# Kernel optimization log

Measured on AMD Instinct MI355X. Metric: run time of the kernel, lower is better.

## Reference

```python
import jax, jax.numpy as jnp
import numpy as np

N, E, IN_DIM, HID, OUT = 50000, 800000, 256, 128, 128
EPS_BN = 1e-5
EPS_NORM = 1e-12


def leaky(x):
    return jnp.where(x >= 0, x, 0.2 * x)


def batchnorm(x, gamma, beta):
    # training-mode BatchNorm1d over node dimension
    mean = jnp.mean(x, axis=0)
    var = jnp.var(x, axis=0)
    return gamma * (x - mean) * jax.lax.rsqrt(var + EPS_BN) + beta


def sage_conv(x, src, dst, W_l, b_l, W_r):
    # PyG SAGEConv (mean aggr): lin_l(mean_{j->i} x_j) + lin_r(x_i)
    msg = x[src]  # [E, D] gather
    agg = jax.ops.segment_sum(msg, dst, num_segments=N)
    cnt = jax.ops.segment_sum(jnp.ones((E,), x.dtype), dst, num_segments=N)
    agg = agg / jnp.maximum(cnt, 1.0)[:, None]
    return agg @ W_l + b_l + x @ W_r


def setup_inputs() -> dict:
    key = jax.random.key(0)
    ks = jax.random.split(key, 16)
    s = lambda fan_in: (2.0 / fan_in) ** 0.5
    return {
        "x": jax.random.normal(ks[0], (N, IN_DIM), jnp.float32),
        "edge_index": jax.random.randint(ks[1], (2, E), 0, N),
        "W_in": jax.random.normal(ks[2], (IN_DIM, HID), jnp.float32) * s(IN_DIM),
        "b_in": jnp.zeros((HID,), jnp.float32),
        "g1": jnp.ones((HID,), jnp.float32),
        "be1": jnp.zeros((HID,), jnp.float32),
        "Wl1": jax.random.normal(ks[3], (HID, HID), jnp.float32) * s(HID),
        "bl1": jnp.zeros((HID,), jnp.float32),
        "Wr1": jax.random.normal(ks[4], (HID, HID), jnp.float32) * s(HID),
        "Wl2": jax.random.normal(ks[5], (HID, OUT), jnp.float32) * s(HID),
        "bl2": jnp.zeros((OUT,), jnp.float32),
        "Wr2": jax.random.normal(ks[6], (HID, OUT), jnp.float32) * s(HID),
        "Wskip": jax.random.normal(ks[7], (HID, OUT), jnp.float32) * s(HID),
        "bskip": jnp.zeros((OUT,), jnp.float32),
        "g2": jnp.ones((OUT,), jnp.float32),
        "be2": jnp.zeros((OUT,), jnp.float32),
    }


def reference(x, edge_index, W_in, b_in, g1, be1, Wl1, bl1, Wr1, Wl2, bl2, Wr2, Wskip, bskip, g2, be2):
    src, dst = edge_index[0], edge_index[1]
    h = batchnorm(leaky(x @ W_in + b_in), g1, be1)
    skip = h
    h1 = leaky(sage_conv(h, src, dst, Wl1, bl1, Wr1))  # dropout = identity (eval)
    h2 = sage_conv(h1, src, dst, Wl2, bl2, Wr2)
    out = h2 + (skip @ Wskip + bskip)
    out = batchnorm(out, g2, be2)
    norm = jnp.sqrt(jnp.sum(out * out, axis=1, keepdims=True))
    return out / jnp.maximum(norm, EPS_NORM)
```

## Files before the change

kernel.cpp:

```cpp
#include <hip/hip_runtime.h>
#include <math.h>

#define N_NODES 50000
#define N_EDGES 800000
#define IN_DIM 256
#define HID 128
#define ZPITCH 384

typedef unsigned short u16;
typedef u16 u16x8 __attribute__((ext_vector_type(8)));
typedef u16 u16x2 __attribute__((ext_vector_type(2)));
typedef __bf16 bf16x8 __attribute__((ext_vector_type(8)));
typedef float f32x4 __attribute__((ext_vector_type(4)));

union F8 { u16x8 u; bf16x8 h; };

__device__ __forceinline__ u16 f2b(float f) {
    unsigned u = __builtin_bit_cast(unsigned, f);
    u = (u + 0x7FFFu + ((u >> 16) & 1u)) >> 16;
    return (u16)u;
}
__device__ __forceinline__ float b2f(u16 h) {
    unsigned u = ((unsigned)h) << 16;
    return __builtin_bit_cast(float, u);
}

template<int A_F32>
__device__ __forceinline__ F8 load_a(const void* base, size_t row, int P, int koff)
{
    F8 r;
    if (A_F32) {
        const float* p = (const float*)base + row * P + koff;
        float4 f0 = *reinterpret_cast<const float4*>(p);
        float4 f1 = *reinterpret_cast<const float4*>(p + 4);
        r.h[0] = (__bf16)f0.x; r.h[1] = (__bf16)f0.y;
        r.h[2] = (__bf16)f0.z; r.h[3] = (__bf16)f0.w;
        r.h[4] = (__bf16)f1.x; r.h[5] = (__bf16)f1.y;
        r.h[6] = (__bf16)f1.z; r.h[7] = (__bf16)f1.w;
    } else {
        r.u = *reinterpret_cast<const u16x8*>((const u16*)base + row * P + koff);
    }
    return r;
}

template<int LEAKY, int STATS, int OUT_BF16, int A_F32, int NC>
__global__ __launch_bounds__(512, 3) void gemm_mfma(
    int M, const void* __restrict__ A, int P,
    const u16* __restrict__ Wf,
    const float* __restrict__ bias0, const float* __restrict__ bias1,
    void* __restrict__ Cout, int CP,
    float* __restrict__ stats)
{
    __shared__ u16 Bs[NC * 4096];

    const int t   = threadIdx.x;
    const int w   = t >> 6;
    const int l   = t & 63;
    const int l15 = l & 15;
    const int lg  = l >> 4;
    const int rb  = blockIdx.x * 128 + w * 16;

    int r0 = rb + l15;
    size_t r0c = (size_t)(r0 < M ? r0 : M - 1);
    const int ko = lg * 8;

    F8 a[NC];
#pragma unroll
    for (int c = 0; c < NC; ++c) a[c] = load_a<A_F32>(A, r0c, P, c * 32 + ko);

#pragma unroll
    for (int i = 0; i < NC; ++i) {
        int idx = i * 512 + t;
        reinterpret_cast<u16x8*>(Bs)[idx] = reinterpret_cast<const u16x8*>(Wf)[idx];
    }
    __syncthreads();

    f32x4 acc[8];
#pragma unroll
    for (int j = 0; j < 8; ++j) acc[j] = 0.0f;

#pragma unroll
    for (int c = 0; c < NC; ++c) {
#pragma unroll
        for (int j = 0; j < 8; ++j) {
            F8 b;
            b.u = reinterpret_cast<const u16x8*>(Bs)[(c * 8 + j) * 64 + l];
            acc[j] = __builtin_amdgcn_mfma_f32_16x16x32_bf16(a[c].h, b.h, acc[j], 0, 0, 0);
        }
    }

    float bias_j[8];
#pragma unroll
    for (int j = 0; j < 8; ++j) {
        float bb = bias0[16 * j + l15];
        if (bias1) bb += bias1[16 * j + l15];
        bias_j[j] = bb;
    }

    float csum[8], csq[8];
#pragma unroll
    for (int j = 0; j < 8; ++j) { csum[j] = 0.f; csq[j] = 0.f; }

    {
        int rbase = rb + lg * 4;
#pragma unroll
        for (int r = 0; r < 4; ++r) {
            int row = rbase + r;
            bool ok = row < M;
#pragma unroll
            for (int j = 0; j < 8; ++j) {
                float y = acc[j][r] + bias_j[j];
                if (LEAKY) y = (y >= 0.f) ? y : 0.2f * y;
                if (ok) {
                    if (OUT_BF16)
                        ((u16*)Cout)[(size_t)row * CP + 16 * j + l15] = f2b(y);
                    else
                        ((float*)Cout)[(size_t)row * CP + 16 * j + l15] = y;
                    if (STATS) { csum[j] += y; csq[j] += y * y; }
                }
            }
        }
    }

    if (STATS) {
        __shared__ float sred[256];
        if (t < 256) sred[t] = 0.f;
        __syncthreads();
#pragma unroll
        for (int j = 0; j < 8; ++j) {
            float s = csum[j];
            float q = csq[j];
            s += __shfl_xor(s, 16); s += __shfl_xor(s, 32);
            q += __shfl_xor(q, 16); q += __shfl_xor(q, 32);
            if (lg == 0) {
                atomicAdd(&sred[16 * j + l15], s);
                atomicAdd(&sred[128 + 16 * j + l15], q);
            }
        }
        __syncthreads();
        if (t < 256) atomicAdd(&stats[t], sred[t]);
    }
}

__global__ __launch_bounds__(256) void conv_w(const float* s0, const float* s1, const float* s2,
                                              const float* sc0, const float* sc1, const float* sc2,
                                              int rows_each, u16* __restrict__ dst, int nchunks)
{
    int tid = blockIdx.x * 256 + threadIdx.x;
    if (tid >= nchunks * 512) return;
    int c   = tid >> 9;
    int j   = (tid >> 6) & 7;
    int l   = tid & 63;
    int l15 = l & 15, lg = l >> 4;

    int srow0 = c * 32;
    int si    = srow0 / rows_each;
    const float* S  = (si == 0) ? s0 : (si == 1) ? s1 : s2;
    const float* SC = (si == 0) ? sc0 : (si == 1) ? sc1 : sc2;
    int rbase = srow0 - si * rows_each + lg * 8;
    int col   = 16 * j + l15;

    u16x8 o;
#pragma unroll
    for (int i = 0; i < 8; ++i) {
        float v = S[(size_t)(rbase + i) * HID + col];
        if (SC) v *= SC[rbase + i];
        o[i] = f2b(v);
    }
    reinterpret_cast<u16x8*>(dst)[tid] = o;
}

__global__ void bias_fold(const float* __restrict__ b0, const float* __restrict__ b1,
                          const float* __restrict__ W0, const float* __restrict__ W1,
                          const float* __restrict__ sh, float* __restrict__ outb)
{
    int j = threadIdx.x;
    float acc = b0[j] + (b1 ? b1[j] : 0.f);
    for (int i = 0; i < HID; ++i) {
        float w = W0[(size_t)i * HID + j] + (W1 ? W1[(size_t)i * HID + j] : 0.f);
        acc = fmaf(sh[i], w, acc);
    }
    outb[j] = acc;
}

__global__ void bn_params(const float* __restrict__ stats,
                          const float* __restrict__ gamma,
                          const float* __restrict__ beta,
                          float* __restrict__ scale,
                          float* __restrict__ shift, float invn)
{
    int j = threadIdx.x;
    float mean = stats[j] * invn;
    float var  = stats[128 + j] * invn - mean * mean;
    var = fmaxf(var, 0.f);
    float sc = gamma[j] / sqrtf(var + 1e-5f);
    scale[j] = sc;
    shift[j] = beta[j] - mean * sc;
}

__global__ __launch_bounds__(256) void edge_count(const int* __restrict__ dst, int* __restrict__ cnt)
{
    int e = blockIdx.x * 256 + threadIdx.x;
    if (e < N_EDGES) atomicAdd(&cnt[dst[e]], 1);
}

__global__ __launch_bounds__(256) void scan_block(const int* __restrict__ cnt,
                                                  int* __restrict__ excl,
                                                  int* __restrict__ bsum, int n)
{
    __shared__ int sh[256];
    int t = threadIdx.x;
    int i = blockIdx.x * 256 + t;
    int v = (i < n) ? cnt[i] : 0;
    sh[t] = v;
    __syncthreads();
#pragma unroll
    for (int off = 1; off < 256; off <<= 1) {
        int x = (t >= off) ? sh[t - off] : 0;
        __syncthreads();
        sh[t] += x;
        __syncthreads();
    }
    if (i < n) excl[i] = sh[t] - v;
    if (t == 255) bsum[blockIdx.x] = sh[255];
}

__global__ __launch_bounds__(256) void scan_bsum(int* __restrict__ bsum, int nb)
{
    __shared__ int sh[256];
    int t = threadIdx.x;
    int v = (t < nb) ? bsum[t] : 0;
    sh[t] = v;
    __syncthreads();
#pragma unroll
    for (int off = 1; off < 256; off <<= 1) {
        int x = (t >= off) ? sh[t - off] : 0;
        __syncthreads();
        sh[t] += x;
        __syncthreads();
    }
    if (t < nb) bsum[t] = sh[t] - v;
}

__global__ __launch_bounds__(256) void scan_add(int* __restrict__ row_ptr,
                                                int* __restrict__ fillrp,
                                                const int* __restrict__ bsum, int n)
{
    int i = blockIdx.x * 256 + threadIdx.x;
    if (i < n) {
        int v = row_ptr[i] + bsum[i >> 8];
        row_ptr[i] = v;
        fillrp[i]  = v;
    }
    if (i == 0) row_ptr[n] = N_EDGES;
}

#define FILL_EPB 4096
__global__ __launch_bounds__(256) void edge_fill_part(const int* __restrict__ src,
                                                      const int* __restrict__ dst,
                                                      int* __restrict__ fillrp,
                                                      int* __restrict__ col_idx)
{
    const int range = blockIdx.x & 7;
    const int base  = (blockIdx.x >> 3) * FILL_EPB;
    const int lo = range * 6250, hi = lo + 6250;
#pragma unroll
    for (int k = 0; k < FILL_EPB / 256; ++k) {
        int e = base + k * 256 + threadIdx.x;
        if (e < N_EDGES) {
            int d = dst[e];
            if (d >= lo && d < hi) {
                int pos = atomicAdd(&fillrp[d], 1);
                col_idx[pos] = src[e];
            }
        }
    }
}

__global__ __launch_bounds__(256) void spmm_mean(const int* __restrict__ row_ptr,
                                                 const int* __restrict__ col_idx,
                                                 const u16* __restrict__ Z_in,
                                                 u16* __restrict__ Z_out)
{
    int node = blockIdx.x * 4 + (threadIdx.x >> 6);
    if (node >= N_NODES) return;
    int lane = threadIdx.x & 63;
    int beg = row_ptr[node];
    int end = row_ptr[node + 1];

    float sx = 0.f, sy = 0.f;
    int e = beg;
    for (; e + 4 <= end; e += 4) {
        int c0 = col_idx[e], c1 = col_idx[e + 1], c2 = col_idx[e + 2], c3 = col_idx[e + 3];
        u16x2 v0 = *reinterpret_cast<const u16x2*>(Z_in + (size_t)c0 * ZPITCH + lane * 2);
        u16x2 v1 = *reinterpret_cast<const u16x2*>(Z_in + (size_t)c1 * ZPITCH + lane * 2);
        u16x2 v2 = *reinterpret_cast<const u16x2*>(Z_in + (size_t)c2 * ZPITCH + lane * 2);
        u16x2 v3 = *reinterpret_cast<const u16x2*>(Z_in + (size_t)c3 * ZPITCH + lane * 2);
        sx += (b2f(v0[0]) + b2f(v1[0])) + (b2f(v2[0]) + b2f(v3[0]));
        sy += (b2f(v0[1]) + b2f(v1[1])) + (b2f(v2[1]) + b2f(v3[1]));
    }
    for (; e < end; ++e) {
        int c = col_idx[e];
        u16x2 v = *reinterpret_cast<const u16x2*>(Z_in + (size_t)c * ZPITCH + lane * 2);
        sx += b2f(v[0]); sy += b2f(v[1]);
    }
    float inv = 1.f / fmaxf((float)(end - beg), 1.f);
    u16x2 r; r[0] = f2b(sx * inv); r[1] = f2b(sy * inv);
    *reinterpret_cast<u16x2*>(Z_out + (size_t)node * ZPITCH + lane * 2) = r;
}

__global__ __launch_bounds__(256) void bn_rownorm(float* __restrict__ out,
                                                  const float* __restrict__ scale,
                                                  const float* __restrict__ shift)
{
    int row = blockIdx.x * 4 + (threadIdx.x >> 6);
    if (row >= N_NODES) return;
    int lane = threadIdx.x & 63;
    float2 v  = *reinterpret_cast<const float2*>(&out[(size_t)row * HID + lane * 2]);
    float2 sc = *reinterpret_cast<const float2*>(&scale[lane * 2]);
    float2 sh = *reinterpret_cast<const float2*>(&shift[lane * 2]);
    float y0 = v.x * sc.x + sh.x;
    float y1 = v.y * sc.y + sh.y;
    float ss = y0 * y0 + y1 * y1;
#pragma unroll
    for (int m = 1; m < 64; m <<= 1) ss += __shfl_xor(ss, m);
    float inv = 1.f / fmaxf(sqrtf(ss), 1e-12f);
    float2 r = {y0 * inv, y1 * inv};
    *reinterpret_cast<float2*>(&out[(size_t)row * HID + lane * 2]) = r;
}

extern "C" void kernel_launch(void* const* d_in, const int* in_sizes, int n_in,
                              void* d_out, int out_size, void* d_ws, size_t ws_size,
                              hipStream_t stream)
{
    const float* x     = (const float*)d_in[0];
    const int*   ei    = (const int*)d_in[1];
    const float* W_in  = (const float*)d_in[2];
    const float* b_in  = (const float*)d_in[3];
    const float* g1    = (const float*)d_in[4];
    const float* be1   = (const float*)d_in[5];
    const float* Wl1   = (const float*)d_in[6];
    const float* bl1   = (const float*)d_in[7];
    const float* Wr1   = (const float*)d_in[8];
    const float* Wl2   = (const float*)d_in[9];
    const float* bl2   = (const float*)d_in[10];
    const float* Wr2   = (const float*)d_in[11];
    const float* Wskip = (const float*)d_in[12];
    const float* bskip = (const float*)d_in[13];
    const float* g2    = (const float*)d_in[14];
    const float* be2   = (const float*)d_in[15];
    float* out = (float*)d_out;

    char* ws = (char*)d_ws;
    u16*  Z  = (u16*)ws;
    char* zzone = ws + 38400000;
    float* stats = (float*)zzone;
    int*   icnt  = (int*)(zzone + 2048);
    size_t zsz   = 2048 + (size_t)N_NODES * 4;
    int*   row_ptr = (int*)(zzone + zsz);
    int*   fillrp  = (int*)(zzone + zsz + 200064);
    int*   bsum    = (int*)(zzone + zsz + 400128);
    int*   col_idx = (int*)(zzone + zsz + 400128 + 1024);
    float* bnc     = (float*)(zzone + zsz + 400128 + 1024 + (size_t)N_EDGES * 4);
    u16* WfA = (u16*)((char*)bnc + 4096);
    u16* WfB = WfA + 8 * 4096;
    u16* WfC = WfB + 8 * 4096;

    hipMemsetAsync(zzone, 0, zsz, stream);

    const int* srcp = ei;
    const int* dstp = ei + N_EDGES;

    float* scale1 = bnc;
    float* shift1 = bnc + 128;
    float* scale2 = bnc + 256;
    float* shift2 = bnc + 384;
    float* b1eff  = bnc + 512;
    float* b2eff  = bnc + 640;

    conv_w<<<16, 256, 0, stream>>>(W_in, nullptr, nullptr, nullptr, nullptr, nullptr,
                                   256, WfA, 8);

    const int NB = (N_NODES + 255) / 256;
    edge_count<<<(N_EDGES + 255) / 256, 256, 0, stream>>>(dstp, icnt);
    scan_block<<<NB, 256, 0, stream>>>(icnt, row_ptr, bsum, N_NODES);
    scan_bsum<<<1, 256, 0, stream>>>(bsum, NB);
    scan_add<<<NB, 256, 0, stream>>>(row_ptr, fillrp, bsum, N_NODES);
    edge_fill_part<<<((N_EDGES + FILL_EPB - 1) / FILL_EPB) * 8, 256, 0, stream>>>(
        srcp, dstp, fillrp, col_idx);

    const int GB = (N_NODES + 127) / 128;

    gemm_mfma<1, 1, 1, 1, 8><<<GB, 512, 0, stream>>>(
        N_NODES, x, IN_DIM, WfA, b_in, nullptr, Z + 128, ZPITCH, stats);
    bn_params<<<1, 128, 0, stream>>>(stats, g1, be1, scale1, shift1, 1.f / N_NODES);

    conv_w<<<16, 256, 0, stream>>>(Wl1, Wr1, nullptr, scale1, scale1, nullptr,
                                   128, WfB, 8);
    conv_w<<<24, 256, 0, stream>>>(Wl2, Wskip, Wr2, nullptr, scale1, nullptr,
                                   128, WfC, 12);
    bias_fold<<<1, 128, 0, stream>>>(bl1, nullptr, Wl1, Wr1, shift1, b1eff);
    bias_fold<<<1, 128, 0, stream>>>(bl2, bskip, Wskip, nullptr, shift1, b2eff);

    spmm_mean<<<(N_NODES + 3) / 4, 256, 0, stream>>>(row_ptr, col_idx, Z + 128, Z);
    gemm_mfma<1, 0, 1, 0, 8><<<GB, 512, 0, stream>>>(
        N_NODES, Z, ZPITCH, WfB, b1eff, nullptr, Z + 256, ZPITCH, nullptr);

    spmm_mean<<<(N_NODES + 3) / 4, 256, 0, stream>>>(row_ptr, col_idx, Z + 256, Z);
    gemm_mfma<0, 1, 0, 0, 12><<<GB, 512, 0, stream>>>(
        N_NODES, Z, ZPITCH, WfC, b2eff, nullptr, out, HID, stats + 256);

    bn_params<<<1, 128, 0, stream>>>(stats + 256, g2, be2, scale2, shift2, 1.f / N_NODES);
    bn_rownorm<<<(N_NODES + 3) / 4, 256, 0, stream>>>(out, scale2, shift2);
}
```

Baseline: 276.2 us.

## Double GEMM rows per wave, async LDS weight load, prefetch A and B fragments

The MFMA GEMM now computes 32 rows per wave (256 per block) so each B fragment read from LDS feeds two MFMAs. Weights are copied into LDS with global_load_lds so they skip registers, A chunks are prefetched a few steps ahead, and the next B fragments are double-buffered in registers. The unused bias1 argument is removed. This raises register pressure (launch bounds lowered to 2 blocks per CU) and halves the grid, which may reduce occupancy and latency hiding.

```diff
diff --git a/kernel.cpp b/kernel.cpp
--- a/kernel.cpp
+++ b/kernel.cpp
@@ -13,6 +13,9 @@
 typedef __bf16 bf16x8 __attribute__((ext_vector_type(8)));
 typedef float f32x4 __attribute__((ext_vector_type(4)));
 
+#define AS1 __attribute__((address_space(1)))
+#define AS3 __attribute__((address_space(3)))
+
 union F8 { u16x8 u; bf16x8 h; };
 
 __device__ __forceinline__ u16 f2b(float f) {
@@ -25,29 +28,46 @@
     return __builtin_bit_cast(float, u);
 }
 
+template<int A_F32> struct ARaw;
+template<> struct ARaw<0> { u16x8 v; };
+template<> struct ARaw<1> { float4 f0, f1; };
+
 template<int A_F32>
-__device__ __forceinline__ F8 load_a(const void* base, size_t row, int P, int koff)
-{
-    F8 r;
-    if (A_F32) {
-        const float* p = (const float*)base + row * P + koff;
-        float4 f0 = *reinterpret_cast<const float4*>(p);
-        float4 f1 = *reinterpret_cast<const float4*>(p + 4);
-        r.h[0] = (__bf16)f0.x; r.h[1] = (__bf16)f0.y;
-        r.h[2] = (__bf16)f0.z; r.h[3] = (__bf16)f0.w;
-        r.h[4] = (__bf16)f1.x; r.h[5] = (__bf16)f1.y;
-        r.h[6] = (__bf16)f1.z; r.h[7] = (__bf16)f1.w;
-    } else {
-        r.u = *reinterpret_cast<const u16x8*>((const u16*)base + row * P + koff);
-    }
+__device__ __forceinline__ ARaw<A_F32> load_raw(const void* base, size_t row, int P, int koff);
+template<>
+__device__ __forceinline__ ARaw<0> load_raw<0>(const void* base, size_t row, int P, int koff) {
+    ARaw<0> r;
+    r.v = *reinterpret_cast<const u16x8*>((const u16*)base + row * P + koff);
     return r;
 }
+template<>
+__device__ __forceinline__ ARaw<1> load_raw<1>(const void* base, size_t row, int P, int koff) {
+    ARaw<1> r;
+    const float* p = (const float*)base + row * P + koff;
+    r.f0 = *reinterpret_cast<const float4*>(p);
+    r.f1 = *reinterpret_cast<const float4*>(p + 4);
+    return r;
+}
+
+template<int A_F32>
+__device__ __forceinline__ F8 to_frag(const ARaw<A_F32>& r);
+template<>
+__device__ __forceinline__ F8 to_frag<0>(const ARaw<0>& r) { F8 f; f.u = r.v; return f; }
+template<>
+__device__ __forceinline__ F8 to_frag<1>(const ARaw<1>& r) {
+    F8 f;
+    f.h[0] = (__bf16)r.f0.x; f.h[1] = (__bf16)r.f0.y;
+    f.h[2] = (__bf16)r.f0.z; f.h[3] = (__bf16)r.f0.w;
+    f.h[4] = (__bf16)r.f1.x; f.h[5] = (__bf16)r.f1.y;
+    f.h[6] = (__bf16)r.f1.z; f.h[7] = (__bf16)r.f1.w;
+    return f;
+}
 
 template<int LEAKY, int STATS, int OUT_BF16, int A_F32, int NC>
-__global__ __launch_bounds__(512, 3) void gemm_mfma(
+__global__ __launch_bounds__(512, 2) void gemm_mfma(
     int M, const void* __restrict__ A, int P,
     const u16* __restrict__ Wf,
-    const float* __restrict__ bias0, const float* __restrict__ bias1,
+    const float* __restrict__ bias0,
     void* __restrict__ Cout, int CP,
     float* __restrict__ stats)
 {
@@ -58,58 +78,84 @@
     const int l   = t & 63;
     const int l15 = l & 15;
     const int lg  = l >> 4;
-    const int rb  = blockIdx.x * 128 + w * 16;
+    const int rb  = blockIdx.x * 256 + w * 32;
 
     int r0 = rb + l15;
+    int r1 = r0 + 16;
     size_t r0c = (size_t)(r0 < M ? r0 : M - 1);
+    size_t r1c = (size_t)(r1 < M ? r1 : M - 1);
     const int ko = lg * 8;
-
-    F8 a[NC];
-#pragma unroll
-    for (int c = 0; c < NC; ++c) a[c] = load_a<A_F32>(A, r0c, P, c * 32 + ko);
 
 #pragma unroll
     for (int i = 0; i < NC; ++i) {
         int idx = i * 512 + t;
-        reinterpret_cast<u16x8*>(Bs)[idx] = reinterpret_cast<const u16x8*>(Wf)[idx];
-    }
+        __builtin_amdgcn_global_load_lds(
+            (const AS1 void*)(Wf + (size_t)idx * 8),
+            (AS3 void*)(Bs + (size_t)idx * 8), 16, 0, 0);
+    }
+
+    constexpr int D = (NC < 4) ? NC : 4;
+    ARaw<A_F32> a0[NC], a1[NC];
+#pragma unroll
+    for (int c = 0; c < D; ++c) {
+        a0[c] = load_raw<A_F32>(A, r0c, P, c * 32 + ko);
+        a1[c] = load_raw<A_F32>(A, r1c, P, c * 32 + ko);
+    }
+
     __syncthreads();
 
-    f32x4 acc[8];
-#pragma unroll
-    for (int j = 0; j < 8; ++j) acc[j] = 0.0f;
+    f32x4 acc[2][8];
+#pragma unroll
+    for (int m = 0; m < 2; ++m)
+#pragma unroll
+        for (int j = 0; j < 8; ++j) acc[m][j] = 0.0f;
+
+    F8 b[8], nb[8];
+#pragma unroll
+    for (int j = 0; j < 8; ++j)
+        b[j].u = *reinterpret_cast<const u16x8*>(Bs + (size_t)(j * 64 + l) * 8);
 
 #pragma unroll
     for (int c = 0; c < NC; ++c) {
+        if (c + D < NC) {
+            a0[c + D] = load_raw<A_F32>(A, r0c, P, (c + D) * 32 + ko);
+            a1[c + D] = load_raw<A_F32>(A, r1c, P, (c + D) * 32 + ko);
+        }
+        if (c + 1 < NC) {
+#pragma unroll
+            for (int j = 0; j < 8; ++j)
+                nb[j].u = *reinterpret_cast<const u16x8*>(
+                    Bs + (size_t)(((c + 1) * 8 + j) * 64 + l) * 8);
+        }
+        F8 fa0 = to_frag<A_F32>(a0[c]);
+        F8 fa1 = to_frag<A_F32>(a1[c]);
 #pragma unroll
         for (int j = 0; j < 8; ++j) {
-            F8 b;
-            b.u = reinterpret_cast<const u16x8*>(Bs)[(c * 8 + j) * 64 + l];
-            acc[j] = __builtin_amdgcn_mfma_f32_16x16x32_bf16(a[c].h, b.h, acc[j], 0, 0, 0);
-        }
+            acc[0][j] = __builtin_amdgcn_mfma_f32_16x16x32_bf16(fa0.h, b[j].h, acc[0][j], 0, 0, 0);
+            acc[1][j] = __builtin_amdgcn_mfma_f32_16x16x32_bf16(fa1.h, b[j].h, acc[1][j], 0, 0, 0);
+        }
+#pragma unroll
+        for (int j = 0; j < 8; ++j) b[j] = nb[j];
     }
 
     float bias_j[8];
 #pragma unroll
-    for (int j = 0; j < 8; ++j) {
-        float bb = bias0[16 * j + l15];
-        if (bias1) bb += bias1[16 * j + l15];
-        bias_j[j] = bb;
-    }
+    for (int j = 0; j < 8; ++j) bias_j[j] = bias0[16 * j + l15];
 
     float csum[8], csq[8];
 #pragma unroll
     for (int j = 0; j < 8; ++j) { csum[j] = 0.f; csq[j] = 0.f; }
 
-    {
-        int rbase = rb + lg * 4;
+#pragma unroll
+    for (int m = 0; m < 2; ++m) {
+        int rbase = rb + m * 16 + lg * 4;
 #pragma unroll
         for (int r = 0; r < 4; ++r) {
             int row = rbase + r;
             bool ok = row < M;
 #pragma unroll
             for (int j = 0; j < 8; ++j) {
-                float y = acc[j][r] + bias_j[j];
+                float y = acc[m][j][r] + bias_j[j];
                 if (LEAKY) y = (y >= 0.f) ? y : 0.2f * y;
                 if (ok) {
                     if (OUT_BF16)
@@ -389,10 +435,10 @@
     edge_fill_part<<<((N_EDGES + FILL_EPB - 1) / FILL_EPB) * 8, 256, 0, stream>>>(
         srcp, dstp, fillrp, col_idx);
 
-    const int GB = (N_NODES + 127) / 128;
+    const int GB = (N_NODES + 255) / 256;
 
     gemm_mfma<1, 1, 1, 1, 8><<<GB, 512, 0, stream>>>(
-        N_NODES, x, IN_DIM, WfA, b_in, nullptr, Z + 128, ZPITCH, stats);
+        N_NODES, x, IN_DIM, WfA, b_in, Z + 128, ZPITCH, stats);
     bn_params<<<1, 128, 0, stream>>>(stats, g1, be1, scale1, shift1, 1.f / N_NODES);
 
     conv_w<<<16, 256, 0, stream>>>(Wl1, Wr1, nullptr, scale1, scale1, nullptr,
@@ -404,11 +450,11 @@
 
     spmm_mean<<<(N_NODES + 3) / 4, 256, 0, stream>>>(row_ptr, col_idx, Z + 128, Z);
     gemm_mfma<1, 0, 1, 0, 8><<<GB, 512, 0, stream>>>(
-        N_NODES, Z, ZPITCH, WfB, b1eff, nullptr, Z + 256, ZPITCH, nullptr);
+        N_NODES, Z, ZPITCH, WfB, b1eff, Z + 256, ZPITCH, nullptr);
 
     spmm_mean<<<(N_NODES + 3) / 4, 256, 0, stream>>>(row_ptr, col_idx, Z + 256, Z);
     gemm_mfma<0, 1, 0, 0, 12><<<GB, 512, 0, stream>>>(
-        N_NODES, Z, ZPITCH, WfC, b2eff, nullptr, out, HID, stats + 256);
+        N_NODES, Z, ZPITCH, WfC, b2eff, out, HID, stats + 256);
 
     bn_params<<<1, 128, 0, stream>>>(stats + 256, g2, be2, scale2, shift2, 1.f / N_NODES);
     bn_rownorm<<<(N_NODES + 3) / 4, 256, 0, stream>>>(out, scale2, shift2);
```

After: 268.6 us. 2.7% less time.
